# Performance work log

Hardware: AMD Instinct MI355X
Metric: run time of the kernel (lower is better)

## Reference

```python
import jax, jax.numpy as jnp
import numpy as np

BLOCK = 32          # QLinearLPBQ block_size
W_BITS = 4          # low-precision blockwise weight quantization
ACT_BITS = 16       # ActivationQDQ(bits=16)


def act_qdq(x):
    # per-tensor symmetric 16-bit fake quant-dequant (dynamic absmax scale)
    qmax = 2.0 ** (ACT_BITS - 1) - 1.0  # 32767
    scale = jnp.maximum(jnp.max(jnp.abs(x)) / qmax, 1e-12)
    return jnp.clip(jnp.round(x / scale), -qmax - 1.0, qmax) * scale


def fixed_qdq_u16(x):
    # FixedActivationQDQ: scale = 1/65536, zero_point = 0, unsigned 16-bit grid
    scale = 1.0 / 65536.0
    return jnp.clip(jnp.round(x / scale), 0.0, 65535.0) * scale


def lpbq_dequant(w):
    # blockwise (per output row, per 32-wide input block) 4-bit fake quant-dequant
    O, I = w.shape
    qmax = 2.0 ** (W_BITS - 1) - 1.0  # 7
    wb = w.reshape(O, I // BLOCK, BLOCK)
    s = jnp.maximum(jnp.max(jnp.abs(wb), axis=-1, keepdims=True) / qmax, 1e-12)
    wq = jnp.clip(jnp.round(wb / s), -qmax - 1.0, qmax) * s
    return wq.reshape(O, I)


def setup_inputs() -> dict:
    key = jax.random.key(0)
    k1, k2, k3, k4 = jax.random.split(key, 4)
    B, S, H, I = 2, 4096, 1024, 3072
    x = jax.random.normal(k1, (B, S, H), jnp.float32)
    w_gate = jax.random.normal(k2, (I, H), jnp.float32) * 0.02
    w_up = jax.random.normal(k3, (I, H), jnp.float32) * 0.02
    w_down = jax.random.normal(k4, (H, I), jnp.float32) * 0.02
    return {"x": x, "w_gate": w_gate, "w_up": w_up, "w_down": w_down}


def reference(x, w_gate, w_up, w_down):
    # x: [B, S, H]
    x = act_qdq(x)                                        # up_proj_input_qdq
    up = act_qdq(x @ lpbq_dequant(w_up).T)                # up_proj + output qdq -> [B,S,I]
    gate = act_qdq(x @ lpbq_dequant(w_gate).T)            # gate_proj + output qdq
    sig = fixed_qdq_u16(jax.nn.sigmoid(gate))             # sigmoid on fixed u16 grid
    gate = act_qdq(gate * sig)                            # SiLU (x*sigmoid) + qdq
    o = act_qdq(gate * up)                                # down_proj_input_qdq
    return o @ lpbq_dequant(w_down).T                     # [B, S, H]
```

## Files before the change

### kernel.cpp

```cpp
#include <hip/hip_runtime.h>
#include <hip/hip_bf16.h>
#include <stdint.h>


#define M_ROWS 8192
#define H_DIM 1024
#define I_DIM 3072

typedef unsigned short u16;
typedef unsigned int u32;
typedef __attribute__((ext_vector_type(8))) short bf16x8;
typedef __attribute__((ext_vector_type(4))) float f32x4;

__device__ __forceinline__ float bf2f(u16 v) { return __uint_as_float(((u32)v) << 16); }
__device__ __forceinline__ u16 f2bf(float f) {
  u32 u = __float_as_uint(f);
  u32 r = (u + 0x7fffu + ((u >> 16) & 1u)) >> 16;
  return (u16)r;
}
__device__ __forceinline__ float qdq16i(float x, float inv, float s) {
  float q = rintf(x * inv);
  q = fminf(fmaxf(q, -32768.f), 32767.f);
  return q * s;
}
__device__ __forceinline__ float sigq(float g) {
  float sig = __builtin_amdgcn_rcpf(1.f + __expf(-g));
  return fminf(fmaxf(rintf(sig * 65536.f), 0.f), 65535.f) * (1.f / 65536.f);
}

__device__ __forceinline__ float scale_read(const u32* __restrict__ scal, int s) {
  u32 m = 0;
#pragma unroll
  for (int j = 0; j < 16; ++j) m = max(m, scal[j * 16 + s]);
  return fmaxf(__uint_as_float(m) / 32767.f, 1e-12f);
}

__device__ __forceinline__ void load_lds16(const u16* g, u16* lds) {
  __builtin_amdgcn_global_load_lds(
      (const __attribute__((address_space(1))) u32*)g,
      (__attribute__((address_space(3))) u32*)lds, 16, 0, 0);
}

__device__ __forceinline__ void block_amax_atomic(float mx, u32* scal, int s) {
#pragma unroll
  for (int off = 32; off; off >>= 1) mx = fmaxf(mx, __shfl_xor(mx, off));
  __shared__ float red[4];
  const int lane = threadIdx.x & 63, wave = threadIdx.x >> 6;
  if (lane == 0) red[wave] = mx;
  __syncthreads();
  if (threadIdx.x == 0) {
    float m = fmaxf(fmaxf(red[0], red[1]), fmaxf(red[2], red[3]));
    atomicMax(scal + (blockIdx.x & 15) * 16 + s, __float_as_uint(m));
  }
}

__device__ __forceinline__ void block_amax2(float a, float b, u32* scal, int sa, int sb) {
#pragma unroll
  for (int off = 32; off; off >>= 1) {
    a = fmaxf(a, __shfl_xor(a, off));
    b = fmaxf(b, __shfl_xor(b, off));
  }
  __shared__ float red2[2][4];
  const int lane = threadIdx.x & 63, wave = threadIdx.x >> 6;
  if (lane == 0) { red2[0][wave] = a; red2[1][wave] = b; }
  __syncthreads();
  if (threadIdx.x == 0) {
    float ma = fmaxf(fmaxf(red2[0][0], red2[0][1]), fmaxf(red2[0][2], red2[0][3]));
    float mb = fmaxf(fmaxf(red2[1][0], red2[1][1]), fmaxf(red2[1][2], red2[1][3]));
    u32* base = scal + (blockIdx.x & 15) * 16;
    atomicMax(base + sa, __float_as_uint(ma));
    atomicMax(base + sb, __float_as_uint(mb));
  }
}

template <int K>
__device__ __forceinline__ void gemm_core(const u16* __restrict__ Ablk,
                                          const u16* __restrict__ Bblk,
                                          f32x4 acc[4][4], u16* smem) {
  u16* As = smem;
  u16* Bs = smem + 4096;
  const int tid = threadIdx.x;
  const int lane = tid & 63, wave = tid >> 6;
  const int wm = wave >> 1, wn = wave & 1;
  const int quad = lane >> 4, mrow = lane & 15;

  const int c0 = tid, c1 = tid + 256;
  const int r0 = c0 >> 2, g0 = ((c0 & 3) ^ ((r0 >> 1) & 3)) * 8;
  const int r1 = c1 >> 2, g1 = ((c1 & 3) ^ ((r1 >> 1) & 3)) * 8;
  const u16* a0 = Ablk + (size_t)r0 * K + g0;
  const u16* a1 = Ablk + (size_t)r1 * K + g1;
  const u16* b0 = Bblk + (size_t)r0 * K + g0;
  const u16* b1 = Bblk + (size_t)r1 * K + g1;
  u16* lA0 = &As[c0 * 8];
  u16* lA1 = &As[c1 * 8];
  u16* lB0 = &Bs[c0 * 8];
  u16* lB1 = &Bs[c1 * 8];

  int aoff[4], boff[4];
  const int lq = (quad ^ ((mrow >> 1) & 3)) * 8;
#pragma unroll
  for (int t = 0; t < 4; ++t) {
    aoff[t] = (wm * 64 + t * 16 + mrow) * 32 + lq;
    boff[t] = (wn * 64 + t * 16 + mrow) * 32 + lq;
  }

  for (int k0 = 0; k0 < K; k0 += 32) {
    __syncthreads();
    load_lds16(a0 + k0, lA0);
    load_lds16(a1 + k0, lA1);
    load_lds16(b0 + k0, lB0);
    load_lds16(b1 + k0, lB1);
    __syncthreads();
    bf16x8 af[4], bfr[4];
#pragma unroll
    for (int t = 0; t < 4; ++t) {
      af[t] = *(const bf16x8*)&As[aoff[t]];
      bfr[t] = *(const bf16x8*)&Bs[boff[t]];
    }
#pragma unroll
    for (int i = 0; i < 4; ++i)
#pragma unroll
      for (int j = 0; j < 4; ++j)
        acc[i][j] = __builtin_amdgcn_mfma_f32_16x16x32_bf16(af[i], bfr[j], acc[i][j], 0, 0, 0);
  }
}

#define HSTRIDE 136

__global__ void __launch_bounds__(256) kgemm1(const u16* __restrict__ xq,
                                              const u16* __restrict__ wcat,
                                              u16* __restrict__ up, u16* __restrict__ gh,
                                              u32* __restrict__ scal) {
  __shared__ __align__(16) u16 smem[8192];
  __shared__ __align__(16) u16 hbuf[128 * HSTRIDE];
  const int tileN = blockIdx.x * 128;
  const int tileM = blockIdx.y * 128;
  const int lane = threadIdx.x & 63, wave = threadIdx.x >> 6;
  const int wm = wave >> 1, wn = wave & 1;
  const int rb = (lane >> 4) * 4, cb = lane & 15;
  const int erow = lane >> 2, echk = lane & 3;
  u16* wbase = smem + wave * 1152;
  const u16* rbase = wbase + erow * 72;
  const u16* Ablk = xq + (size_t)tileM * H_DIM;
  f32x4 acc[4][4];

#pragma unroll
  for (int i = 0; i < 4; ++i)
#pragma unroll
    for (int j = 0; j < 4; ++j) acc[i][j] = (f32x4){0.f, 0.f, 0.f, 0.f};
  gemm_core<H_DIM>(Ablk, wcat + (size_t)(I_DIM + tileN) * H_DIM, acc, smem);
  {
    float mxg = 0.f, mxh = 0.f;
#pragma unroll
    for (int i = 0; i < 4; ++i) {
      __syncthreads();
#pragma unroll
      for (int j = 0; j < 4; ++j)
#pragma unroll
        for (int r = 0; r < 4; ++r) {
          float g = acc[i][j][r];
          mxg = fmaxf(mxg, fabsf(g));
          wbase[(rb + r) * 72 + j * 16 + cb] = f2bf(g);
          float ha = g * sigq(g);
          mxh = fmaxf(mxh, fabsf(ha));
          hbuf[(wm * 64 + i * 16 + rb + r) * HSTRIDE + wn * 64 + j * 16 + cb] = f2bf(ha);
        }
      __syncthreads();
      uint4 v0 = *(const uint4*)(rbase + echk * 8);
      uint4 v1 = *(const uint4*)(rbase + (echk + 4) * 8);
      size_t grow = (size_t)(tileM + wm * 64 + i * 16 + erow) * I_DIM + (tileN + wn * 64);
      *(uint4*)(gh + grow + echk * 8) = v0;
      *(uint4*)(gh + grow + (echk + 4) * 8) = v1;
    }
    block_amax2(mxg, mxh, scal, 2, 3);
  }

#pragma unroll
  for (int i = 0; i < 4; ++i)
#pragma unroll
    for (int j = 0; j < 4; ++j) acc[i][j] = (f32x4){0.f, 0.f, 0.f, 0.f};
  gemm_core<H_DIM>(Ablk, wcat + (size_t)tileN * H_DIM, acc, smem);
  {
    float mxu = 0.f, mxo = 0.f;
#pragma unroll
    for (int i = 0; i < 4; ++i) {
      __syncthreads();
#pragma unroll
      for (int j = 0; j < 4; ++j)
#pragma unroll
        for (int r = 0; r < 4; ++r) {
          float u = acc[i][j][r];
          mxu = fmaxf(mxu, fabsf(u));
          wbase[(rb + r) * 72 + j * 16 + cb] = f2bf(u);
          float ha = bf2f(hbuf[(wm * 64 + i * 16 + rb + r) * HSTRIDE + wn * 64 + j * 16 + cb]);
          mxo = fmaxf(mxo, fabsf(ha * u));
        }
      __syncthreads();
      uint4 v0 = *(const uint4*)(rbase + echk * 8);
      uint4 v1 = *(const uint4*)(rbase + (echk + 4) * 8);
      size_t grow = (size_t)(tileM + wm * 64 + i * 16 + erow) * I_DIM + (tileN + wn * 64);
      *(uint4*)(up + grow + echk * 8) = v0;
      *(uint4*)(up + grow + (echk + 4) * 8) = v1;
    }
    block_amax2(mxu, mxo, scal, 1, 4);
  }
}

__global__ void __launch_bounds__(256) kgemm2(const u16* __restrict__ oq,
                                              const u16* __restrict__ wdq,
                                              float* __restrict__ out) {
  __shared__ __align__(16) u16 smem[8192];
  const int tileN = blockIdx.x * 128;
  const int tileM = blockIdx.y * 128;
  f32x4 acc[4][4];
#pragma unroll
  for (int i = 0; i < 4; ++i)
#pragma unroll
    for (int j = 0; j < 4; ++j) acc[i][j] = (f32x4){0.f, 0.f, 0.f, 0.f};
  gemm_core<I_DIM>(oq + (size_t)tileM * I_DIM, wdq + (size_t)tileN * I_DIM, acc, smem);

  const int lane = threadIdx.x & 63, wave = threadIdx.x >> 6;
  const int wm = wave >> 1, wn = wave & 1;
  const int rb = (lane >> 4) * 4, cb = lane & 15;
#pragma unroll
  for (int i = 0; i < 4; ++i) {
#pragma unroll
    for (int j = 0; j < 4; ++j) {
      size_t base = (size_t)(tileM + wm * 64 + i * 16 + rb) * H_DIM +
                    (size_t)(tileN + wn * 64 + j * 16 + cb);
#pragma unroll
      for (int r = 0; r < 4; ++r) out[base + (size_t)r * H_DIM] = acc[i][j][r];
    }
  }
}

__global__ void __launch_bounds__(256) kprep(const float* __restrict__ x,
                                             const float* __restrict__ wu,
                                             const float* __restrict__ wg,
                                             const float* __restrict__ wdn,
                                             u16* __restrict__ wcat, u16* __restrict__ wdq,
                                             u32* __restrict__ scal) {
  if (blockIdx.x < 1024) {
    const float4* x4 = (const float4*)x;
    const int n4 = (M_ROWS * H_DIM) / 4;
    float mx = 0.f;
    for (int i = blockIdx.x * 256 + threadIdx.x; i < n4; i += 1024 * 256) {
      float4 v = x4[i];
      mx = fmaxf(fmaxf(fabsf(v.x), fabsf(v.y)), fmaxf(fmaxf(fabsf(v.z), fabsf(v.w)), mx));
    }
    block_amax_atomic(mx, scal, 0);
    return;
  }
  const int gid = (blockIdx.x - 1024) * 256 + threadIdx.x;
  const int unit = gid >> 3, l8 = gid & 7;
  const float* src;
  u16* dst;
  int u;
  if (unit < 98304)       { src = wu;  dst = wcat;            u = unit; }
  else if (unit < 196608) { src = wg;  dst = wcat + 3145728;  u = unit - 98304; }
  else                    { src = wdn; dst = wdq;             u = unit - 196608; }
  const size_t off = (size_t)u * 32 + (size_t)l8 * 4;
  float4 v = *(const float4*)(src + off);
  float m = fmaxf(fmaxf(fabsf(v.x), fabsf(v.y)), fmaxf(fabsf(v.z), fabsf(v.w)));
  m = fmaxf(m, __shfl_xor(m, 1));
  m = fmaxf(m, __shfl_xor(m, 2));
  m = fmaxf(m, __shfl_xor(m, 4));
  const float s = fmaxf(m / 7.0f, 1e-12f);
  const float inv = 1.0f / s;
  float vv[4] = {v.x, v.y, v.z, v.w};
  u16 o[4];
#pragma unroll
  for (int e = 0; e < 4; ++e) {
    float q = rintf(vv[e] * inv);
    q = fminf(fmaxf(q, -8.f), 7.f);
    o[e] = f2bf(q * s);
  }
  *(ushort4*)(dst + off) = make_ushort4(o[0], o[1], o[2], o[3]);
}

__global__ void __launch_bounds__(256) kqdqx(const float4* __restrict__ x,
                                             ushort4* __restrict__ xq,
                                             const u32* __restrict__ scal) {
  const float s = scale_read(scal, 0);
  const float inv = 1.0f / s;
  const int i = blockIdx.x * 256 + threadIdx.x;
  float4 v = x[i];
  ushort4 o;
  o.x = f2bf(qdq16i(v.x, inv, s));
  o.y = f2bf(qdq16i(v.y, inv, s));
  o.z = f2bf(qdq16i(v.z, inv, s));
  o.w = f2bf(qdq16i(v.w, inv, s));
  xq[i] = o;
}

#define GH4 ((M_ROWS * I_DIM) / 8)
#define EW_BLOCKS 2048

__global__ void __launch_bounds__(256) kmulo(uint4* __restrict__ gh, const uint4* __restrict__ up,
                                             u32* __restrict__ scal) {
  const float sg = scale_read(scal, 2), ig = 1.0f / sg;
  const float sh = scale_read(scal, 3), ih = 1.0f / sh;
  const float su = scale_read(scal, 1), iu = 1.0f / su;
  const float so = scale_read(scal, 4), io = 1.0f / so;
  for (int i = blockIdx.x * 256 + threadIdx.x; i < GH4; i += EW_BLOCKS * 256) {
    union { uint4 v; u16 us[8]; } a, b;
    a.v = gh[i];
    b.v = up[i];
#pragma unroll
    for (int e = 0; e < 8; ++e) {
      float g = qdq16i(bf2f(a.us[e]), ig, sg);
      float h = g * sigq(g);
      float o = qdq16i(h, ih, sh) * qdq16i(bf2f(b.us[e]), iu, su);
      a.us[e] = f2bf(qdq16i(o, io, so));
    }
    gh[i] = a.v;
  }
}

extern "C" void kernel_launch(void* const* d_in, const int* in_sizes, int n_in,
                              void* d_out, int out_size, void* d_ws, size_t ws_size,
                              hipStream_t stream) {
  (void)in_sizes; (void)n_in; (void)out_size; (void)ws_size;
  const float* x   = (const float*)d_in[0];
  const float* wg  = (const float*)d_in[1];
  const float* wu  = (const float*)d_in[2];
  const float* wdn = (const float*)d_in[3];
  float* out = (float*)d_out;
  char* ws = (char*)d_ws;

  u32* scal = (u32*)ws;
  u16* xq   = (u16*)(ws + 1024);
  u16* wcat = xq + (size_t)M_ROWS * H_DIM;
  u16* wdq  = wcat + (size_t)2 * I_DIM * H_DIM;
  u16* up   = wdq + (size_t)H_DIM * I_DIM;
  u16* gh   = up + (size_t)M_ROWS * I_DIM;

  hipMemsetAsync(scal, 0, 1024, stream);
  kprep<<<1024 + 9216, 256, 0, stream>>>(x, wu, wg, wdn, wcat, wdq, scal);
  kqdqx<<<(M_ROWS * H_DIM) / 4 / 256, 256, 0, stream>>>((const float4*)x, (ushort4*)xq, scal);
  kgemm1<<<dim3(24, 64), 256, 0, stream>>>(xq, wcat, up, gh, scal);
  kmulo<<<EW_BLOCKS, 256, 0, stream>>>((uint4*)gh, (const uint4*)up, scal);
  kgemm2<<<dim3(8, 64), 256, 0, stream>>>(gh, wdq, out);
}
```

Before: 349.0 us.

## Split gate/up GEMM across blocks, split-K down GEMM with atomics, separate amax pass

The fused gate+up GEMM kernel is split so each block computes only one projection tile, doubling the grid and removing the large hbuf shared buffer. The h and o absmax values, previously computed in the GEMM epilogue, now come from a new elementwise pass (kamaxho) that rereads gh and up. The down-projection GEMM uses a 3-way split-K over a 24x64 grid, accumulating into a zeroed output with float atomicAdd. These changes are meant to raise parallelism and occupancy. In exchange they add an extra full read of the intermediates, a memset of the output, atomic traffic, and a nondeterministic summation order.

```diff
diff --git a/kernel.cpp b/kernel.cpp
--- a/kernel.cpp
+++ b/kernel.cpp
@@ -73,10 +73,10 @@
   }
 }
 
-template <int K>
+template <int KSTRIDE>
 __device__ __forceinline__ void gemm_core(const u16* __restrict__ Ablk,
                                           const u16* __restrict__ Bblk,
-                                          f32x4 acc[4][4], u16* smem) {
+                                          int klen, f32x4 acc[4][4], u16* smem) {
   u16* As = smem;
   u16* Bs = smem + 4096;
   const int tid = threadIdx.x;
@@ -87,10 +87,10 @@
   const int c0 = tid, c1 = tid + 256;
   const int r0 = c0 >> 2, g0 = ((c0 & 3) ^ ((r0 >> 1) & 3)) * 8;
   const int r1 = c1 >> 2, g1 = ((c1 & 3) ^ ((r1 >> 1) & 3)) * 8;
-  const u16* a0 = Ablk + (size_t)r0 * K + g0;
-  const u16* a1 = Ablk + (size_t)r1 * K + g1;
-  const u16* b0 = Bblk + (size_t)r0 * K + g0;
-  const u16* b1 = Bblk + (size_t)r1 * K + g1;
+  const u16* a0 = Ablk + (size_t)r0 * KSTRIDE + g0;
+  const u16* a1 = Ablk + (size_t)r1 * KSTRIDE + g1;
+  const u16* b0 = Bblk + (size_t)r0 * KSTRIDE + g0;
+  const u16* b1 = Bblk + (size_t)r1 * KSTRIDE + g1;
   u16* lA0 = &As[c0 * 8];
   u16* lA1 = &As[c1 * 8];
   u16* lB0 = &Bs[c0 * 8];
@@ -104,7 +104,7 @@
     boff[t] = (wn * 64 + t * 16 + mrow) * 32 + lq;
   }
 
-  for (int k0 = 0; k0 < K; k0 += 32) {
+  for (int k0 = 0; k0 < klen; k0 += 32) {
     __syncthreads();
     load_lds16(a0 + k0, lA0);
     load_lds16(a1 + k0, lA1);
@@ -125,99 +125,69 @@
   }
 }
 
-#define HSTRIDE 136
-
 __global__ void __launch_bounds__(256) kgemm1(const u16* __restrict__ xq,
                                               const u16* __restrict__ wcat,
                                               u16* __restrict__ up, u16* __restrict__ gh,
                                               u32* __restrict__ scal) {
   __shared__ __align__(16) u16 smem[8192];
-  __shared__ __align__(16) u16 hbuf[128 * HSTRIDE];
   const int tileN = blockIdx.x * 128;
   const int tileM = blockIdx.y * 128;
+  f32x4 acc[4][4];
+#pragma unroll
+  for (int i = 0; i < 4; ++i)
+#pragma unroll
+    for (int j = 0; j < 4; ++j) acc[i][j] = (f32x4){0.f, 0.f, 0.f, 0.f};
+  gemm_core<H_DIM>(xq + (size_t)tileM * H_DIM, wcat + (size_t)tileN * H_DIM,
+                   H_DIM, acc, smem);
+
+  u16* outp;
+  int ncol, slot;
+  if (tileN < I_DIM) { outp = up; ncol = tileN; slot = 1; }
+  else               { outp = gh; ncol = tileN - I_DIM; slot = 2; }
+
   const int lane = threadIdx.x & 63, wave = threadIdx.x >> 6;
   const int wm = wave >> 1, wn = wave & 1;
   const int rb = (lane >> 4) * 4, cb = lane & 15;
   const int erow = lane >> 2, echk = lane & 3;
   u16* wbase = smem + wave * 1152;
   const u16* rbase = wbase + erow * 72;
-  const u16* Ablk = xq + (size_t)tileM * H_DIM;
-  f32x4 acc[4][4];
-
-#pragma unroll
-  for (int i = 0; i < 4; ++i)
-#pragma unroll
-    for (int j = 0; j < 4; ++j) acc[i][j] = (f32x4){0.f, 0.f, 0.f, 0.f};
-  gemm_core<H_DIM>(Ablk, wcat + (size_t)(I_DIM + tileN) * H_DIM, acc, smem);
-  {
-    float mxg = 0.f, mxh = 0.f;
-#pragma unroll
-    for (int i = 0; i < 4; ++i) {
-      __syncthreads();
-#pragma unroll
-      for (int j = 0; j < 4; ++j)
-#pragma unroll
-        for (int r = 0; r < 4; ++r) {
-          float g = acc[i][j][r];
-          mxg = fmaxf(mxg, fabsf(g));
-          wbase[(rb + r) * 72 + j * 16 + cb] = f2bf(g);
-          float ha = g * sigq(g);
-          mxh = fmaxf(mxh, fabsf(ha));
-          hbuf[(wm * 64 + i * 16 + rb + r) * HSTRIDE + wn * 64 + j * 16 + cb] = f2bf(ha);
-        }
-      __syncthreads();
-      uint4 v0 = *(const uint4*)(rbase + echk * 8);
-      uint4 v1 = *(const uint4*)(rbase + (echk + 4) * 8);
-      size_t grow = (size_t)(tileM + wm * 64 + i * 16 + erow) * I_DIM + (tileN + wn * 64);
-      *(uint4*)(gh + grow + echk * 8) = v0;
-      *(uint4*)(gh + grow + (echk + 4) * 8) = v1;
-    }
-    block_amax2(mxg, mxh, scal, 2, 3);
-  }
-
-#pragma unroll
-  for (int i = 0; i < 4; ++i)
-#pragma unroll
-    for (int j = 0; j < 4; ++j) acc[i][j] = (f32x4){0.f, 0.f, 0.f, 0.f};
-  gemm_core<H_DIM>(Ablk, wcat + (size_t)tileN * H_DIM, acc, smem);
-  {
-    float mxu = 0.f, mxo = 0.f;
-#pragma unroll
-    for (int i = 0; i < 4; ++i) {
-      __syncthreads();
-#pragma unroll
-      for (int j = 0; j < 4; ++j)
-#pragma unroll
-        for (int r = 0; r < 4; ++r) {
-          float u = acc[i][j][r];
-          mxu = fmaxf(mxu, fabsf(u));
-          wbase[(rb + r) * 72 + j * 16 + cb] = f2bf(u);
-          float ha = bf2f(hbuf[(wm * 64 + i * 16 + rb + r) * HSTRIDE + wn * 64 + j * 16 + cb]);
-          mxo = fmaxf(mxo, fabsf(ha * u));
-        }
-      __syncthreads();
-      uint4 v0 = *(const uint4*)(rbase + echk * 8);
-      uint4 v1 = *(const uint4*)(rbase + (echk + 4) * 8);
-      size_t grow = (size_t)(tileM + wm * 64 + i * 16 + erow) * I_DIM + (tileN + wn * 64);
-      *(uint4*)(up + grow + echk * 8) = v0;
-      *(uint4*)(up + grow + (echk + 4) * 8) = v1;
-    }
-    block_amax2(mxu, mxo, scal, 1, 4);
-  }
+  float mx = 0.f;
+#pragma unroll
+  for (int i = 0; i < 4; ++i) {
+    __syncthreads();
+#pragma unroll
+    for (int j = 0; j < 4; ++j)
+#pragma unroll
+      for (int r = 0; r < 4; ++r) {
+        float v = acc[i][j][r];
+        mx = fmaxf(mx, fabsf(v));
+        wbase[(rb + r) * 72 + j * 16 + cb] = f2bf(v);
+      }
+    __syncthreads();
+    uint4 v0 = *(const uint4*)(rbase + echk * 8);
+    uint4 v1 = *(const uint4*)(rbase + (echk + 4) * 8);
+    size_t grow = (size_t)(tileM + wm * 64 + i * 16 + erow) * I_DIM + (ncol + wn * 64);
+    *(uint4*)(outp + grow + echk * 8) = v0;
+    *(uint4*)(outp + grow + (echk + 4) * 8) = v1;
+  }
+  block_amax_atomic(mx, scal, slot);
 }
 
 __global__ void __launch_bounds__(256) kgemm2(const u16* __restrict__ oq,
                                               const u16* __restrict__ wdq,
                                               float* __restrict__ out) {
   __shared__ __align__(16) u16 smem[8192];
-  const int tileN = blockIdx.x * 128;
+  const int tileN = (blockIdx.x & 7) * 128;
+  const int ksplit = blockIdx.x >> 3;
+  const int koff = ksplit * 1024;
   const int tileM = blockIdx.y * 128;
   f32x4 acc[4][4];
 #pragma unroll
   for (int i = 0; i < 4; ++i)
 #pragma unroll
     for (int j = 0; j < 4; ++j) acc[i][j] = (f32x4){0.f, 0.f, 0.f, 0.f};
-  gemm_core<I_DIM>(oq + (size_t)tileM * I_DIM, wdq + (size_t)tileN * I_DIM, acc, smem);
+  gemm_core<I_DIM>(oq + (size_t)tileM * I_DIM + koff,
+                   wdq + (size_t)tileN * I_DIM + koff, 1024, acc, smem);
 
   const int lane = threadIdx.x & 63, wave = threadIdx.x >> 6;
   const int wm = wave >> 1, wn = wave & 1;
@@ -229,7 +199,7 @@
       size_t base = (size_t)(tileM + wm * 64 + i * 16 + rb) * H_DIM +
                     (size_t)(tileN + wn * 64 + j * 16 + cb);
 #pragma unroll
-      for (int r = 0; r < 4; ++r) out[base + (size_t)r * H_DIM] = acc[i][j][r];
+      for (int r = 0; r < 4; ++r) atomicAdd(&out[base + (size_t)r * H_DIM], acc[i][j][r]);
     }
   }
 }
@@ -296,6 +266,27 @@
 #define GH4 ((M_ROWS * I_DIM) / 8)
 #define EW_BLOCKS 2048
 
+__global__ void __launch_bounds__(256) kamaxho(const uint4* __restrict__ gh,
+                                               const uint4* __restrict__ up,
+                                               u32* __restrict__ scal) {
+  const float sg = scale_read(scal, 2), ig = 1.0f / sg;
+  const float su = scale_read(scal, 1), iu = 1.0f / su;
+  float mxh = 0.f, mxo = 0.f;
+  for (int i = blockIdx.x * 256 + threadIdx.x; i < GH4; i += EW_BLOCKS * 256) {
+    union { uint4 v; u16 us[8]; } a, b;
+    a.v = gh[i];
+    b.v = up[i];
+#pragma unroll
+    for (int e = 0; e < 8; ++e) {
+      float g = qdq16i(bf2f(a.us[e]), ig, sg);
+      float h = g * sigq(g);
+      mxh = fmaxf(mxh, fabsf(h));
+      mxo = fmaxf(mxo, fabsf(h * qdq16i(bf2f(b.us[e]), iu, su)));
+    }
+  }
+  block_amax2(mxh, mxo, scal, 3, 4);
+}
+
 __global__ void __launch_bounds__(256) kmulo(uint4* __restrict__ gh, const uint4* __restrict__ up,
                                              u32* __restrict__ scal) {
   const float sg = scale_read(scal, 2), ig = 1.0f / sg;
@@ -336,9 +327,11 @@
   u16* gh   = up + (size_t)M_ROWS * I_DIM;
 
   hipMemsetAsync(scal, 0, 1024, stream);
+  hipMemsetAsync(out, 0, (size_t)M_ROWS * H_DIM * 4, stream);
   kprep<<<1024 + 9216, 256, 0, stream>>>(x, wu, wg, wdn, wcat, wdq, scal);
   kqdqx<<<(M_ROWS * H_DIM) / 4 / 256, 256, 0, stream>>>((const float4*)x, (ushort4*)xq, scal);
-  kgemm1<<<dim3(24, 64), 256, 0, stream>>>(xq, wcat, up, gh, scal);
+  kgemm1<<<dim3(48, 64), 256, 0, stream>>>(xq, wcat, up, gh, scal);
+  kamaxho<<<EW_BLOCKS, 256, 0, stream>>>((const uint4*)gh, (const uint4*)up, scal);
   kmulo<<<EW_BLOCKS, 256, 0, stream>>>((uint4*)gh, (const uint4*)up, scal);
-  kgemm2<<<dim3(8, 64), 256, 0, stream>>>(gh, wdq, out);
-}
+  kgemm2<<<dim3(24, 64), 256, 0, stream>>>(gh, wdq, out);
+}
```

Result: slower. 430.8 us (+23.4%).
